# Performance work log

Measured on AMD Instinct MI355X. Metric: run time of the kernel, lower is better.

## Reference

```python
import jax, jax.numpy as jnp
import numpy as np

EPS_COS = 1e-8   # nxn_cos_sim eps
SMOOTH = 1e-4    # DiceLoss smooth
EPS_DICE = 1e-7  # smp soft_dice_score clamp_min eps

BS, C, H, W = 8, 512, 128, 128
K = 512  # codebook / num classes


def setup_inputs() -> dict:
    key = jax.random.key(0)
    k1, k2, k3 = jax.random.split(key, 3)
    output = jax.random.normal(k1, (BS, C, H, W), dtype=jnp.float32)
    embeddings = jax.random.normal(k2, (K, C), dtype=jnp.float32)
    # ground-truth one-hot annotation (bs, K, h, w)
    gt_labels = jax.random.randint(k3, (BS, H, W), 0, K)
    ann_one_hot = jax.nn.one_hot(gt_labels, K, dtype=jnp.float32).transpose(0, 3, 1, 2)
    return {"output": output, "ann_one_hot": ann_one_hot, "embeddings": embeddings}


def reference(output, ann_one_hot, embeddings):
    bs, c, h, w = output.shape
    k = embeddings.shape[0]
    x = output.transpose(0, 2, 3, 1).reshape(-1, c)           # [N, C]
    # nxn cosine similarity [N, K]
    numerator = x @ embeddings.T
    a_l2 = jnp.sum(x * x, axis=1)                              # [N]
    b_l2 = jnp.sum(embeddings * embeddings, axis=1)            # [K]
    denominator = jnp.maximum(jnp.sqrt(a_l2[:, None] * b_l2[None, :]), EPS_COS)
    labels = jnp.argmax(numerator / denominator, axis=-1).reshape(bs, h, w)
    # ann_to_one_hot -> (bs, K, h, w)
    pred_one_hot = jax.nn.one_hot(labels, k, dtype=output.dtype).transpose(0, 3, 1, 2)
    # smp DiceLoss(mode='multilabel', smooth=1e-4, from_logits=False)
    yp = pred_one_hot.reshape(bs, k, -1)
    yt = ann_one_hot.reshape(bs, k, -1).astype(yp.dtype)
    dims = (0, 2)
    intersection = jnp.sum(yp * yt, axis=dims)                 # [K]
    cardinality = jnp.sum(yp + yt, axis=dims)                  # [K]
    score = (2.0 * intersection + SMOOTH) / jnp.maximum(cardinality + SMOOTH, EPS_DICE)
    loss = 1.0 - score
    present = (jnp.sum(yt, axis=dims) > 0).astype(loss.dtype)  # only classes present in GT
    return jnp.mean(loss * present)
```

## Files before the change

### kernel.cpp

```cpp
#include <hip/hip_runtime.h>
#include <hip/hip_bf16.h>

#define BSZ 8
#define CDIM 512
#define KDIM 512
#define HWSZ 16384
#define NPIX (BSZ*HWSZ)

using bf16x8 = __attribute__((ext_vector_type(8))) short;
using f32x4  = __attribute__((ext_vector_type(4))) float;
typedef unsigned long long u64;

__device__ __forceinline__ unsigned pack2bf16(float lo, float hi) {
  return (__builtin_bit_cast(unsigned, lo) >> 16) |
         (__builtin_bit_cast(unsigned, hi) & 0xFFFF0000u);
}

__device__ __forceinline__ void gload_lds16(const unsigned short* g, unsigned short* l) {
  __builtin_amdgcn_global_load_lds(
      (const __attribute__((address_space(1))) unsigned int*)g,
      (__attribute__((address_space(3))) unsigned int*)l, 16, 0, 0);
}

__global__ __launch_bounds__(64) void prep_emb_kernel(const float* __restrict__ E,
                                                      unsigned short* __restrict__ Eb,
                                                      unsigned short* __restrict__ EbT) {
  int k = blockIdx.x;
  int lane = threadIdx.x;
  const float4* row = (const float4*)(E + (size_t)k * CDIM);
  float4 v0 = row[lane * 2], v1 = row[lane * 2 + 1];
  float ss = v0.x*v0.x + v0.y*v0.y + v0.z*v0.z + v0.w*v0.w
           + v1.x*v1.x + v1.y*v1.y + v1.z*v1.z + v1.w*v1.w;
  #pragma unroll
  for (int d = 1; d < 64; d <<= 1) ss += __shfl_xor(ss, d, 64);
  float rinv = rsqrtf(fmaxf(ss, 1e-24f));
  float f[8] = {v0.x, v0.y, v0.z, v0.w, v1.x, v1.y, v1.z, v1.w};
  unsigned o[8];
  #pragma unroll
  for (int e = 0; e < 8; ++e) {
    float x = f[e] * rinv;
    unsigned u = __builtin_bit_cast(unsigned, x);
    o[e] = (u + 0x7FFFu + ((u >> 16) & 1u)) >> 16;
  }
  uint4 pack;
  pack.x = o[0] | (o[1] << 16);
  pack.y = o[2] | (o[3] << 16);
  pack.z = o[4] | (o[5] << 16);
  pack.w = o[6] | (o[7] << 16);
  ((uint4*)(Eb + (size_t)k * CDIM))[lane] = pack;
  int clsb = k >> 7, rowi = k & 127, cs = lane >> 2, q4 = lane & 3;
  *(uint4*)(EbT + (size_t)clsb * 65536 + cs * 4096 + rowi * 32 + q4 * 8) = pack;
}

__global__ __launch_bounds__(256) void transpose_gt_kernel(
    const float* __restrict__ X, const float* __restrict__ ANN,
    unsigned short* __restrict__ XtT, float* __restrict__ gt_count) {
  __shared__ unsigned int lds[256 * 36];
  __shared__ float swr[4];
  int t = threadIdx.x;
  int bid = blockIdx.x;
  int pt = bid & 511, cg = bid >> 9;
  int px0 = pt * 256, c0 = cg * 64;
  int b = px0 >> 14, hw = px0 & (HWSZ - 1);
  int w = t >> 6, lane = t & 63;

  const float* xb = X + ((size_t)b * CDIM + c0 + 16 * w) * HWSZ + hw + 4 * lane;
  const float* Ap = ANN + (size_t)bid * HWSZ + 4 * t;
  float s0 = 0.f;

  #pragma unroll
  for (int ph = 0; ph < 2; ++ph) {
    float4 xv[8];
    #pragma unroll
    for (int r = 0; r < 4; ++r) {
      int cc = 2 * (4 * ph + r);
      xv[2*r]   = *(const float4*)(xb + (size_t)cc * HWSZ);
      xv[2*r+1] = *(const float4*)(xb + (size_t)(cc + 1) * HWSZ);
    }
    #pragma unroll
    for (int r = 0; r < 8; ++r) {
      float4 a4 = *(const float4*)(Ap + (size_t)(8 * ph + r) * 1024);
      s0 += (a4.x + a4.y) + (a4.z + a4.w);
    }
    #pragma unroll
    for (int j = 0; j < 4; ++j) {
      unsigned pk[4];
      #pragma unroll
      for (int r = 0; r < 4; ++r)
        pk[r] = pack2bf16(((const float*)&xv[2*r])[j], ((const float*)&xv[2*r+1])[j]);
      *(uint4*)&lds[(size_t)(4 * lane + j) * 36 + 8 * w + 4 * ph] = *(const uint4*)pk;
    }
  }
  __syncthreads();
  #pragma unroll
  for (int rr = 0; rr < 8; ++rr) {
    int ch = rr * 256 + t;
    int q4 = ch & 3, px = (ch >> 2) & 255, s = ch >> 10;
    uint4 o = *(const uint4*)&lds[(size_t)px * 36 + s * 16 + q4 * 4];
    int pxg = px0 + px;
    int pxb = pxg >> 7, prow = pxg & 127;
    int ics = cg * 2 + s;
    *(uint4*)(XtT + (size_t)(pxb * 16 + ics) * 4096 + prow * 32 + q4 * 8) = o;
  }
  #pragma unroll
  for (int d = 1; d < 64; d <<= 1) s0 += __shfl_xor(s0, d, 64);
  if (lane == 0) swr[w] = s0;
  __syncthreads();
  if (t == 0) atomicAdd(&gt_count[bid & (KDIM - 1)], swr[0] + swr[1] + swr[2] + swr[3]);
}

__global__ __launch_bounds__(256, 4) void gemm_argmax_kernel(
    const unsigned short* __restrict__ XtT, const unsigned short* __restrict__ EbT,
    u64* __restrict__ keys) {
  __shared__ unsigned short As[2][128 * 32];
  __shared__ unsigned short Bs[2][128 * 32];
  int t = threadIdx.x;
  int lane = t & 63;
  int wv = t >> 6;
  int p15 = lane & 15, q = lane >> 4;
  int wr = wv >> 1, wc = wv & 1;
  int bid = (blockIdx.x & 7) * 512 + (blockIdx.x >> 3);
  int pxb  = bid >> 2;
  int clsb = bid & 3;
  int px0  = pxb * 128;
  int cls0 = clsb * 128;

  const unsigned short* Abase = XtT + (size_t)pxb * 65536;
  const unsigned short* Bbase = EbT + (size_t)clsb * 65536;
  int ubase = (t & ~63) * 8;
  #define STAGE(buf, i)                                                       \
    {                                                                         \
      _Pragma("unroll")                                                       \
      for (int j = 0; j < 2; ++j) {                                           \
        int ch = t + 256 * j;                                                 \
        gload_lds16(Abase + (size_t)(i) * 4096 + ch * 8, &As[buf][ubase + j * 2048]); \
        gload_lds16(Bbase + (size_t)(i) * 4096 + ch * 8, &Bs[buf][ubase + j * 2048]); \
      }                                                                       \
    }

  f32x4 acc[4][4];
  #pragma unroll
  for (int m = 0; m < 4; ++m)
    #pragma unroll
    for (int n = 0; n < 4; ++n)
      acc[m][n] = (f32x4){0.f, 0.f, 0.f, 0.f};

  STAGE(0, 0);
  for (int i = 0; i < 16; ++i) {
    int cur = i & 1;
    if (i < 15) STAGE(cur ^ 1, i + 1);
    __syncthreads();
    bf16x8 a[4], bfr[4];
    #pragma unroll
    for (int m = 0; m < 4; ++m)
      a[m] = *(bf16x8*)&As[cur][(wr * 64 + m * 16 + p15) * 32 + q * 8];
    #pragma unroll
    for (int n = 0; n < 4; ++n)
      bfr[n] = *(bf16x8*)&Bs[cur][(wc * 64 + n * 16 + p15) * 32 + q * 8];
    #pragma unroll
    for (int n = 0; n < 4; ++n)
      #pragma unroll
      for (int m = 0; m < 4; ++m)
        acc[m][n] = __builtin_amdgcn_mfma_f32_16x16x32_bf16(a[m], bfr[n], acc[m][n], 0, 0, 0);
    __syncthreads();
  }
  #undef STAGE

  #pragma unroll
  for (int m = 0; m < 4; ++m) {
    #pragma unroll
    for (int r = 0; r < 4; ++r) {
      float best = acc[m][0][r];
      int bn = 0;
      #pragma unroll
      for (int n = 1; n < 4; ++n) {
        float v = acc[m][n][r];
        if (v > best) { best = v; bn = n; }
      }
      int bk = cls0 + wc * 64 + bn * 16 + p15;
      #pragma unroll
      for (int d = 1; d < 16; d <<= 1) {
        float ov = __shfl_xor(best, d, 64);
        int   ok = __shfl_xor(bk, d, 64);
        if (ov > best || (ov == best && ok < bk)) { best = ov; bk = ok; }
      }
      if (p15 == 0) {
        int px = px0 + wr * 64 + m * 16 + q * 4 + r;
        unsigned u = __builtin_bit_cast(unsigned, best);
        unsigned ou = u ^ ((unsigned)((int)u >> 31) | 0x80000000u);
        u64 key = ((u64)ou << 32) | (unsigned)(511 - bk);
        atomicMax(&keys[px], key);
      }
    }
  }
}

__global__ __launch_bounds__(256) void count_kernel(
    const u64* __restrict__ keys, const float* __restrict__ ANN,
    int* __restrict__ pred_count, int* __restrict__ inter) {
  int px = blockIdx.x * 256 + threadIdx.x;
  u64 key = keys[px];
  int cls = 511 - (int)(unsigned)(key & 0xFFFFFFFFull);
  atomicAdd(&pred_count[cls], 1);
  int b = px >> 14, hw = px & (HWSZ - 1);
  float g = ANN[((size_t)b * KDIM + cls) * HWSZ + hw];
  if (g > 0.5f) atomicAdd(&inter[cls], 1);
}

__global__ __launch_bounds__(512) void final_kernel(
    const int* __restrict__ pred_count, const int* __restrict__ inter,
    const float* __restrict__ gt_count, float* __restrict__ out) {
  int k = threadIdx.x;
  float G = gt_count[k];
  float P = (float)pred_count[k];
  float I = (float)inter[k];
  float card  = P + G;
  float score = (2.f * I + 1e-4f) / fmaxf(card + 1e-4f, 1e-7f);
  float v = (G > 0.f) ? (1.f - score) : 0.f;
  #pragma unroll
  for (int d = 1; d < 64; d <<= 1) v += __shfl_xor(v, d, 64);
  __shared__ float sw[8];
  if ((k & 63) == 0) sw[k >> 6] = v;
  __syncthreads();
  if (k == 0) {
    float s = 0.f;
    #pragma unroll
    for (int i = 0; i < 8; ++i) s += sw[i];
    out[0] = s / (float)KDIM;
  }
}

__global__ __launch_bounds__(256) void gt_count_fb(const float* __restrict__ ANN,
                                                   float* __restrict__ gt_count) {
  int slice = blockIdx.x;
  int k = slice & (KDIM - 1);
  const float4* p = (const float4*)(ANN + (size_t)slice * HWSZ);
  float s = 0.f;
  #pragma unroll
  for (int i = 0; i < 16; ++i) {
    float4 v = p[threadIdx.x + i * 256];
    s += v.x + v.y + v.z + v.w;
  }
  #pragma unroll
  for (int d = 1; d < 64; d <<= 1) s += __shfl_xor(s, d, 64);
  __shared__ float sw[4];
  if ((threadIdx.x & 63) == 0) sw[threadIdx.x >> 6] = s;
  __syncthreads();
  if (threadIdx.x == 0) atomicAdd(&gt_count[k], sw[0] + sw[1] + sw[2] + sw[3]);
}

__global__ __launch_bounds__(256, 1) void gemm_fb(
    const float* __restrict__ X, const float* __restrict__ ANN,
    const unsigned short* __restrict__ Eb,
    int* __restrict__ pred_count, int* __restrict__ inter) {
  int tid = threadIdx.x;
  int wv = tid >> 6;
  int lane = tid & 63;
  int p15 = lane & 15, q = lane >> 4;
  int pix0 = blockIdx.x * 64;
  int b = pix0 >> 14;
  int hw = pix0 & (HWSZ - 1);
  const float*          Xb = X  + (size_t)b * CDIM * HWSZ + hw + p15;
  const unsigned short* Ew = Eb + (size_t)(wv * 128) * CDIM;
  f32x4 acc[4][8];
  #pragma unroll
  for (int m = 0; m < 4; ++m)
    #pragma unroll
    for (int n = 0; n < 8; ++n)
      acc[m][n] = (f32x4){0.f, 0.f, 0.f, 0.f};
  for (int cs = 0; cs < 16; ++cs) {
    int c0 = cs * 32 + q * 8;
    bf16x8 a[4];
    #pragma unroll
    for (int m = 0; m < 4; ++m)
      #pragma unroll
      for (int e = 0; e < 8; ++e) {
        float x = Xb[(size_t)(c0 + e) * HWSZ + m * 16];
        a[m][e] = (short)(__builtin_bit_cast(unsigned, x) >> 16);
      }
    bf16x8 bfrag[8];
    #pragma unroll
    for (int n = 0; n < 8; ++n)
      bfrag[n] = *(const bf16x8*)(Ew + (size_t)(n * 16 + p15) * CDIM + cs * 32 + q * 8);
    #pragma unroll
    for (int n = 0; n < 8; ++n)
      #pragma unroll
      for (int m = 0; m < 4; ++m)
        acc[m][n] = __builtin_amdgcn_mfma_f32_16x16x32_bf16(a[m], bfrag[n], acc[m][n], 0, 0, 0);
  }
  __shared__ float s_v[4][64];
  __shared__ int   s_k[4][64];
  #pragma unroll
  for (int m = 0; m < 4; ++m)
    #pragma unroll
    for (int r = 0; r < 4; ++r) {
      float best = acc[m][0][r];
      int bn = 0;
      #pragma unroll
      for (int n = 1; n < 8; ++n) {
        float v = acc[m][n][r];
        if (v > best) { best = v; bn = n; }
      }
      int bk = wv * 128 + bn * 16 + p15;
      #pragma unroll
      for (int d = 1; d < 16; d <<= 1) {
        float ov = __shfl_xor(best, d, 64);
        int   ok = __shfl_xor(bk, d, 64);
        if (ov > best || (ov == best && ok < bk)) { best = ov; bk = ok; }
      }
      if (p15 == 0) {
        int p = m * 16 + q * 4 + r;
        s_v[wv][p] = best;
        s_k[wv][p] = bk;
      }
    }
  __syncthreads();
  if (tid < 64) {
    int p = tid;
    float best = s_v[0][p]; int bk = s_k[0][p];
    #pragma unroll
    for (int w = 1; w < 4; ++w) {
      float v = s_v[w][p]; int kk = s_k[w][p];
      if (v > best || (v == best && kk < bk)) { best = v; bk = kk; }
    }
    atomicAdd(&pred_count[bk], 1);
    float g = ANN[((size_t)b * KDIM + bk) * HWSZ + hw + p];
    if (g > 0.5f) atomicAdd(&inter[bk], 1);
  }
}

extern "C" void kernel_launch(void* const* d_in, const int* in_sizes, int n_in,
                              void* d_out, int out_size, void* d_ws, size_t ws_size,
                              hipStream_t stream) {
  const float* X   = (const float*)d_in[0];
  const float* ANN = (const float*)d_in[1];
  const float* E   = (const float*)d_in[2];

  char* base = (char*)d_ws;
  unsigned short* Eb  = (unsigned short*)base;
  unsigned short* EbT = (unsigned short*)(base + 524288);
  float* gt_count     = (float*)(base + 1048576);
  int*   pred_count   = (int*)  (base + 1048576 + 2048);
  int*   inter        = (int*)  (base + 1048576 + 4096);
  u64*   keys         = (u64*)  (base + 1048576 + 8192);
  unsigned short* XtT = (unsigned short*)(base + 4194304);

  size_t need = 4194304 + (size_t)NPIX * CDIM * 2;

  prep_emb_kernel<<<KDIM, 64, 0, stream>>>(E, Eb, EbT);
  if (ws_size >= need) {
    hipMemsetAsync(base + 1048576, 0, 8192 + 1048576, stream);
    transpose_gt_kernel<<<4096, 256, 0, stream>>>(X, ANN, XtT, gt_count);
    gemm_argmax_kernel<<<4096, 256, 0, stream>>>(XtT, EbT, keys);
    count_kernel<<<NPIX / 256, 256, 0, stream>>>(keys, ANN, pred_count, inter);
  } else {
    hipMemsetAsync(base + 1048576, 0, 6144, stream);
    gt_count_fb<<<BSZ * KDIM, 256, 0, stream>>>(ANN, gt_count);
    gemm_fb<<<NPIX / 64, 256, 0, stream>>>(X, ANN, Eb, pred_count, inter);
  }
  final_kernel<<<1, 512, 0, stream>>>(pred_count, inter, gt_count, (float*)d_out);
}
```

Measured before the change: 277.5 us.

## Split GT counting from transpose and widen transpose tiles with swizzled LDS

The fused transpose+GT-count kernel is split into a standalone GT-count reduction kernel and a new transpose kernel. Each transpose block now handles 1024 pixels by 32 channels, using an XOR-swizzled LDS layout, and writes full 16-channel slabs of the bf16 XtT layout. The goal is better coalescing and fewer bank conflicts in the transpose, at the cost of one extra kernel launch and a separate pass over the annotation tensor. Each thread now holds 32 float4 registers, so register pressure and occupancy may suffer.

```diff
diff --git a/kernel.cpp b/kernel.cpp
--- a/kernel.cpp
+++ b/kernel.cpp
@@ -52,61 +52,74 @@
   *(uint4*)(EbT + (size_t)clsb * 65536 + cs * 4096 + rowi * 32 + q4 * 8) = pack;
 }
 
-__global__ __launch_bounds__(256) void transpose_gt_kernel(
-    const float* __restrict__ X, const float* __restrict__ ANN,
-    unsigned short* __restrict__ XtT, float* __restrict__ gt_count) {
-  __shared__ unsigned int lds[256 * 36];
-  __shared__ float swr[4];
-  int t = threadIdx.x;
+__global__ __launch_bounds__(256) void gt_count_kernel(const float* __restrict__ ANN,
+                                                       float* __restrict__ gt_count) {
+  int slice = blockIdx.x;
+  int k = slice & (KDIM - 1);
+  const float4* p = (const float4*)(ANN + (size_t)slice * HWSZ);
+  float s = 0.f;
+  #pragma unroll
+  for (int i = 0; i < 16; ++i) {
+    float4 v = p[threadIdx.x + i * 256];
+    s += v.x + v.y + v.z + v.w;
+  }
+  #pragma unroll
+  for (int d = 1; d < 64; d <<= 1) s += __shfl_xor(s, d, 64);
+  __shared__ float sw[4];
+  if ((threadIdx.x & 63) == 0) sw[threadIdx.x >> 6] = s;
+  __syncthreads();
+  if (threadIdx.x == 0) {
+    atomicAdd(&gt_count[k], sw[0] + sw[1] + sw[2] + sw[3]);
+  }
+}
+
+__global__ __launch_bounds__(256) void transpose_v3_kernel(
+    const float* __restrict__ X, unsigned short* __restrict__ XtT) {
+  __shared__ unsigned int lds[16 * 1024];
+  int t = threadIdx.x, w = t >> 6, l = t & 63;
   int bid = blockIdx.x;
-  int pt = bid & 511, cg = bid >> 9;
-  int px0 = pt * 256, c0 = cg * 64;
+  int pt = bid >> 4, ks = bid & 15;
+  int px0 = pt << 10;
   int b = px0 >> 14, hw = px0 & (HWSZ - 1);
-  int w = t >> 6, lane = t & 63;
-
-  const float* xb = X + ((size_t)b * CDIM + c0 + 16 * w) * HWSZ + hw + 4 * lane;
-  const float* Ap = ANN + (size_t)bid * HWSZ + 4 * t;
-  float s0 = 0.f;
-
-  #pragma unroll
-  for (int ph = 0; ph < 2; ++ph) {
-    float4 xv[8];
-    #pragma unroll
-    for (int r = 0; r < 4; ++r) {
-      int cc = 2 * (4 * ph + r);
-      xv[2*r]   = *(const float4*)(xb + (size_t)cc * HWSZ);
-      xv[2*r+1] = *(const float4*)(xb + (size_t)(cc + 1) * HWSZ);
-    }
-    #pragma unroll
-    for (int r = 0; r < 8; ++r) {
-      float4 a4 = *(const float4*)(Ap + (size_t)(8 * ph + r) * 1024);
-      s0 += (a4.x + a4.y) + (a4.z + a4.w);
-    }
+  const float* xb = X + ((size_t)b * CDIM + ks * 32 + 8 * w) * HWSZ + hw + 4 * l;
+
+  float4 xv[8][4];
+  #pragma unroll
+  for (int r = 0; r < 8; ++r)
+    #pragma unroll
+    for (int s = 0; s < 4; ++s)
+      xv[r][s] = *(const float4*)(xb + (size_t)r * HWSZ + s * 256);
+
+  #pragma unroll
+  for (int rp = 0; rp < 4; ++rp) {
+    int cp = 4 * w + rp;
+    int swz = (cp & 7) << 2;
+    #pragma unroll
+    for (int s = 0; s < 4; ++s) {
+      unsigned pk[4];
+      #pragma unroll
+      for (int j = 0; j < 4; ++j)
+        pk[j] = pack2bf16(((const float*)&xv[2 * rp][s])[j],
+                          ((const float*)&xv[2 * rp + 1][s])[j]);
+      *(uint4*)&lds[cp * 1024 + ((s * 256 + 4 * l) ^ swz)] = *(const uint4*)pk;
+    }
+  }
+  __syncthreads();
+
+  #pragma unroll
+  for (int rr = 0; rr < 16; ++rr) {
+    int ch = rr * 256 + t;
+    int q4 = ch & 3, pxl = ch >> 2;
+    unsigned o[4];
     #pragma unroll
     for (int j = 0; j < 4; ++j) {
-      unsigned pk[4];
-      #pragma unroll
-      for (int r = 0; r < 4; ++r)
-        pk[r] = pack2bf16(((const float*)&xv[2*r])[j], ((const float*)&xv[2*r+1])[j]);
-      *(uint4*)&lds[(size_t)(4 * lane + j) * 36 + 8 * w + 4 * ph] = *(const uint4*)pk;
-    }
-  }
-  __syncthreads();
-  #pragma unroll
-  for (int rr = 0; rr < 8; ++rr) {
-    int ch = rr * 256 + t;
-    int q4 = ch & 3, px = (ch >> 2) & 255, s = ch >> 10;
-    uint4 o = *(const uint4*)&lds[(size_t)px * 36 + s * 16 + q4 * 4];
-    int pxg = px0 + px;
-    int pxb = pxg >> 7, prow = pxg & 127;
-    int ics = cg * 2 + s;
-    *(uint4*)(XtT + (size_t)(pxb * 16 + ics) * 4096 + prow * 32 + q4 * 8) = o;
-  }
-  #pragma unroll
-  for (int d = 1; d < 64; d <<= 1) s0 += __shfl_xor(s0, d, 64);
-  if (lane == 0) swr[w] = s0;
-  __syncthreads();
-  if (t == 0) atomicAdd(&gt_count[bid & (KDIM - 1)], swr[0] + swr[1] + swr[2] + swr[3]);
+      int cp = 4 * q4 + j;
+      o[j] = lds[cp * 1024 + (pxl ^ ((cp & 7) << 2))];
+    }
+    int pxg = px0 + pxl;
+    *(uint4*)(XtT + ((size_t)(pxg >> 7) * 16 + ks) * 4096 + (size_t)(pxg & 127) * 32 + q4 * 8)
+        = *(const uint4*)o;
+  }
 }
 
 __global__ __launch_bounds__(256, 4) void gemm_argmax_kernel(
@@ -230,25 +243,6 @@
   }
 }
 
-__global__ __launch_bounds__(256) void gt_count_fb(const float* __restrict__ ANN,
-                                                   float* __restrict__ gt_count) {
-  int slice = blockIdx.x;
-  int k = slice & (KDIM - 1);
-  const float4* p = (const float4*)(ANN + (size_t)slice * HWSZ);
-  float s = 0.f;
-  #pragma unroll
-  for (int i = 0; i < 16; ++i) {
-    float4 v = p[threadIdx.x + i * 256];
-    s += v.x + v.y + v.z + v.w;
-  }
-  #pragma unroll
-  for (int d = 1; d < 64; d <<= 1) s += __shfl_xor(s, d, 64);
-  __shared__ float sw[4];
-  if ((threadIdx.x & 63) == 0) sw[threadIdx.x >> 6] = s;
-  __syncthreads();
-  if (threadIdx.x == 0) atomicAdd(&gt_count[k], sw[0] + sw[1] + sw[2] + sw[3]);
-}
-
 __global__ __launch_bounds__(256, 1) void gemm_fb(
     const float* __restrict__ X, const float* __restrict__ ANN,
     const unsigned short* __restrict__ Eb,
@@ -350,12 +344,13 @@
   prep_emb_kernel<<<KDIM, 64, 0, stream>>>(E, Eb, EbT);
   if (ws_size >= need) {
     hipMemsetAsync(base + 1048576, 0, 8192 + 1048576, stream);
-    transpose_gt_kernel<<<4096, 256, 0, stream>>>(X, ANN, XtT, gt_count);
+    gt_count_kernel<<<BSZ * KDIM, 256, 0, stream>>>(ANN, gt_count);
+    transpose_v3_kernel<<<2048, 256, 0, stream>>>(X, XtT);
     gemm_argmax_kernel<<<4096, 256, 0, stream>>>(XtT, EbT, keys);
     count_kernel<<<NPIX / 256, 256, 0, stream>>>(keys, ANN, pred_count, inter);
   } else {
     hipMemsetAsync(base + 1048576, 0, 6144, stream);
-    gt_count_fb<<<BSZ * KDIM, 256, 0, stream>>>(ANN, gt_count);
+    gt_count_kernel<<<BSZ * KDIM, 256, 0, stream>>>(ANN, gt_count);
     gemm_fb<<<NPIX / 64, 256, 0, stream>>>(X, ANN, Eb, pred_count, inter);
   }
   final_kernel<<<1, 512, 0, stream>>>(pred_count, inter, gt_count, (float*)d_out);
```

Result: slower. 289.1 us (+4.2%).
